# Kernel optimization log

Hardware: AMD Instinct MI355X
Metric: run time of the kernel (lower is better)

## Reference

```python
import jax, jax.numpy as jnp
import numpy as np

NUM_TEAMS = 200000
EMBED_DIM = 16
NUM_EDGES = 3200000
BATCH = 500000
EPS_NORM = 1e-12  # F.normalize clamp
EPS_SOFTMAX = 1e-16  # PyG edge-softmax denom eps
NEG_SLOPE = 0.01  # LeakyReLU default


def setup_inputs() -> dict:
    key = jax.random.key(0)
    ks = jax.random.split(key, 12)
    inp = {}
    inp["embed"] = jax.random.normal(ks[0], (NUM_TEAMS, EMBED_DIM), dtype=jnp.float32)
    inp["beta"] = jnp.ones((2,), dtype=jnp.float32)  # one learnable scalar per AGNNConv
    # torch Linear init ~ U(-1/sqrt(fan_in), 1/sqrt(fan_in)); stored as [in, out]
    def lin(k, fi, fo):
        b = 1.0 / np.sqrt(fi)
        k1, k2 = jax.random.split(k)
        return (jax.random.uniform(k1, (fi, fo), jnp.float32, -b, b),
                jax.random.uniform(k2, (fo,), jnp.float32, -b, b))
    inp["lin0_w"], inp["lin0_b"] = lin(ks[1], 2 * EMBED_DIM, 6)
    inp["lin1_w"], inp["lin1_b"] = lin(ks[2], 6, 16)
    inp["lin2_w"], inp["lin2_b"] = lin(ks[3], 16, 3)
    inp["edge_index"] = jax.random.randint(ks[4], (2, NUM_EDGES), 0, NUM_TEAMS, dtype=jnp.int64)
    inp["home"] = jax.random.randint(ks[5], (BATCH,), 0, NUM_TEAMS, dtype=jnp.int64)
    inp["away"] = jax.random.randint(ks[6], (BATCH,), 0, NUM_TEAMS, dtype=jnp.int64)
    return inp


def _agnn_conv(x, beta, src, dst, n):
    # x: [N, D]; messages flow src(j) -> dst(i); scatter-softmax over edges per dst
    xn = x / jnp.maximum(jnp.linalg.norm(x, axis=-1, keepdims=True), EPS_NORM)
    alpha = beta * jnp.sum(xn[src] * xn[dst], axis=-1)          # [E]
    m = jax.ops.segment_max(alpha, dst, num_segments=n)          # [N]
    a = jnp.exp(alpha - m[dst])                                   # [E]
    denom = jax.ops.segment_sum(a, dst, num_segments=n)          # [N]
    a = a / (denom[dst] + EPS_SOFTMAX)
    return jax.ops.segment_sum(a[:, None] * x[src], dst, num_segments=n)  # [N, D]


def _forward(embed, beta, lin0_w, lin0_b, lin1_w, lin1_b, lin2_w, lin2_b,
             src, dst, home, away):
    n = embed.shape[0]
    act = lambda v: jax.nn.leaky_relu(v, NEG_SLOPE)
    x = embed  # embedding of arange(n_teams) == the table itself
    x = act(_agnn_conv(x, beta[0], src, dst, n))
    x = act(_agnn_conv(x, beta[1], src, dst, n))
    h = jnp.concatenate([x[home], x[away]], axis=-1)  # [B, 2D]
    h = act(h @ lin0_w + lin0_b)
    h = act(h @ lin1_w + lin1_b)
    h = act(h @ lin2_w + lin2_b)
    return jax.nn.log_softmax(h, axis=0).reshape(-1, 3)  # LogSoftmax(dim=0), faithful


def reference(embed, beta, lin0_w, lin0_b, lin1_w, lin1_b, lin2_w, lin2_b,
              edge_index, home, away):
    n = embed.shape[0]
    # AGNNConv default: remove then add self-loops
    loops = jnp.arange(n, dtype=edge_index.dtype)
    mask = edge_index[0] != edge_index[1]
    safe = jnp.where(mask, edge_index[1], edge_index[0])  # self-loop-out non-loop edges
    src = jnp.concatenate([edge_index[0], loops])
    dst = jnp.concatenate([jnp.where(mask, edge_index[1], edge_index[0]), loops])
    # masked self-loops in original list become src==dst duplicates of the appended
    # self-loops only if random collision; to faithfully *remove* them we redirect
    # removed edges onto the node's own appended self-loop (alpha identical for
    # src==dst), which changes only duplicate self-loop counts with prob ~1/N.
    return _forward(embed, beta, lin0_w, lin0_b, lin1_w, lin1_b, lin2_w, lin2_b,
                    src, dst, home, away)
```

## Files before the change

### kernel.cpp

```cpp
#include <hip/hip_runtime.h>
#include <hip/hip_fp16.h>
#include <math.h>

#define TPB 256
#define NPB 512
#define NPB_SHIFT 9
#define EPB 8192
#define EPW 16
#define BCAP 12288
#define RSTRIDE 32

typedef float v2f __attribute__((ext_vector_type(2)));

__device__ __forceinline__ float leaky_relu(float v) { return v > 0.0f ? v : 0.01f * v; }

__device__ __forceinline__ float dot4(float4 a, float4 b) {
    return a.x * b.x + a.y * b.y + a.z * b.z + a.w * b.w;
}
__device__ __forceinline__ float4 f4_scale(float4 a, float s) {
    return make_float4(a.x * s, a.y * s, a.z * s, a.w * s);
}
__device__ __forceinline__ float4 f4_acc(float4 a, float w, float4 y) {
    return make_float4(fmaf(w, y.x, a.x), fmaf(w, y.y, a.y),
                       fmaf(w, y.z, a.z), fmaf(w, y.w, a.w));
}
__device__ __forceinline__ float4 f4_add_shfl(float4 v, int d) {
    return make_float4(v.x + __shfl_xor(v.x, d, 64), v.y + __shfl_xor(v.y, d, 64),
                       v.z + __shfl_xor(v.z, d, 64), v.w + __shfl_xor(v.w, d, 64));
}
__device__ __forceinline__ float4 leaky4(float4 v) {
    return make_float4(leaky_relu(v.x), leaky_relu(v.y), leaky_relu(v.z), leaky_relu(v.w));
}

__device__ __forceinline__ float4 dec4(unsigned w) {
    v2f lo = __builtin_amdgcn_cvt_pk_f32_fp8((int)w, false);
    v2f hi = __builtin_amdgcn_cvt_pk_f32_fp8((int)w, true);
    return make_float4(lo.x, lo.y, hi.x, hi.y);
}
__device__ __forceinline__ unsigned enc4(float4 v) {
    int r = __builtin_amdgcn_cvt_pk_fp8_f32(v.x, v.y, 0, false);
    r = __builtin_amdgcn_cvt_pk_fp8_f32(v.z, v.w, r, true);
    return (unsigned)r;
}

__device__ __forceinline__ void store_h4(__half* row, int l, float4 v) {
    union { float2 f; __half h[4]; } u;
    u.h[0] = __float2half(v.x); u.h[1] = __float2half(v.y);
    u.h[2] = __float2half(v.z); u.h[3] = __float2half(v.w);
    ((float2*)row)[l] = u.f;
}

__device__ __forceinline__ uint4 rec_q(const char* base, int i) {
    return *(const uint4*)(base + (size_t)i * RSTRIDE);
}
__device__ __forceinline__ float rec_n(const char* base, int i) {
    return *(const float*)(base + (size_t)i * RSTRIDE + 16);
}

__device__ __forceinline__ int wave_incl_scan(int v, int lane) {
#pragma unroll
    for (int off = 1; off < 64; off <<= 1) {
        int u = __shfl_up(v, off, 64);
        if (lane >= off) v += u;
    }
    return v;
}

__global__ void k_binA(const int* __restrict__ src, const int* __restrict__ dst,
                       unsigned* __restrict__ bdata, int* __restrict__ cbase,
                       int* __restrict__ ccnt, int E, int K,
                       const float* __restrict__ x, char* __restrict__ xqn,
                       int N) {
    __shared__ int hist[512];
    __shared__ unsigned lcol[EPB];
    __shared__ int wsum[8];
    int t = threadIdx.x;
    int lane = t & 63, wv = t >> 6;
    int c = blockIdx.x;
    int e0 = c * EPB;
    int e1 = min(e0 + EPB, E);
    int tot = e1 - e0;
    hist[t] = 0;
    __syncthreads();
    int myd[EPW], mys[EPW];
    if (tot == EPB) {
        const int4* d4 = (const int4*)(dst + e0);
        const int4* s4 = (const int4*)(src + e0);
#pragma unroll
        for (int k = 0; k < 4; ++k) {
            int4 dd = d4[t + k * 512];
            int4 ss = s4[t + k * 512];
            myd[4 * k + 0] = dd.x; myd[4 * k + 1] = dd.y;
            myd[4 * k + 2] = dd.z; myd[4 * k + 3] = dd.w;
            mys[4 * k + 0] = ss.x; mys[4 * k + 1] = ss.y;
            mys[4 * k + 2] = ss.z; mys[4 * k + 3] = ss.w;
            atomicAdd(&hist[dd.x >> NPB_SHIFT], 1);
            atomicAdd(&hist[dd.y >> NPB_SHIFT], 1);
            atomicAdd(&hist[dd.z >> NPB_SHIFT], 1);
            atomicAdd(&hist[dd.w >> NPB_SHIFT], 1);
        }
    } else {
#pragma unroll
        for (int k = 0; k < EPW; ++k) {
            int e = e0 + t + k * 512;
            int d = (e < e1) ? dst[e] : -1;
            mys[k] = (e < e1) ? src[e] : 0;
            myd[k] = d;
            if (d >= 0) atomicAdd(&hist[d >> NPB_SHIFT], 1);
        }
    }
    __syncthreads();
    int v = hist[t];
    int inc = wave_incl_scan(v, lane);
    if (lane == 63) wsum[wv] = inc;
    __syncthreads();
    if (t == 0) {
        int acc = 0;
#pragma unroll
        for (int k = 0; k < 8; ++k) { int xv = wsum[k]; wsum[k] = acc; acc += xv; }
    }
    __syncthreads();
    int excl = inc + wsum[wv] - v;
    if (t < K) {
        cbase[(size_t)c * K + t] = excl;
        ccnt[(size_t)c * K + t] = v;
    }
    __syncthreads();
    hist[t] = excl;
    __syncthreads();
    if (tot == EPB) {
#pragma unroll
        for (int k = 0; k < EPW; ++k) {
            int d = myd[k];
            int p = atomicAdd(&hist[d >> NPB_SHIFT], 1);
            lcol[p] = ((unsigned)(d & (NPB - 1)) << 18) | (unsigned)mys[k];
        }
    } else {
#pragma unroll
        for (int k = 0; k < EPW; ++k) {
            int d = myd[k];
            if (d >= 0) {
                int p = atomicAdd(&hist[d >> NPB_SHIFT], 1);
                lcol[p] = ((unsigned)(d & (NPB - 1)) << 18) | (unsigned)mys[k];
            }
        }
    }
    __syncthreads();
    unsigned* outp = bdata + (size_t)c * EPB;
    for (int i = t; i < tot; i += 512) outp[i] = lcol[i];
    int i = c * 512 + t;
    if (i < N) {
        const float4* xp = (const float4*)(x + (size_t)i * 16);
        float4 a = xp[0], b = xp[1], cc = xp[2], d = xp[3];
        float ss = dot4(a, a) + dot4(b, b) + dot4(cc, cc) + dot4(d, d);
        float nn = fmaxf(sqrtf(ss), 1e-12f);
        float inv = 1.0f / nn;
        char* rp = xqn + (size_t)i * RSTRIDE;
        *(uint4*)rp = make_uint4(enc4(f4_scale(a, inv)), enc4(f4_scale(b, inv)),
                                 enc4(f4_scale(cc, inv)), enc4(f4_scale(d, inv)));
        *(float*)(rp + 16) = nn;
    }
}

__global__ void k_binB(const unsigned* __restrict__ bdata, const int* __restrict__ cbase,
                       const int* __restrict__ ccnt,
                       int2* __restrict__ rng,
                       int* __restrict__ col, int N, int NC, int K) {
    __shared__ int cb[512];
    __shared__ int cc[512];
    __shared__ int ldeg[NPB];
    __shared__ int wsum[8];
    int b = blockIdx.x, t = threadIdx.x;
    int lane = t & 63, wv = t >> 6;
    int n0 = b << NPB_SHIFT;
    int nn = min(NPB, N - n0);
    cb[t] = (t < NC) ? cbase[(size_t)t * K + b] : 0;
    cc[t] = (t < NC) ? ccnt[(size_t)t * K + b] : 0;
    ldeg[t] = 0;
    __syncthreads();
    int mycnt = (t < NC) ? cc[t] : 0;
    const unsigned* myp = bdata + (size_t)t * EPB + cb[t];
    for (int k = 0; k < mycnt; ++k) {
        unsigned e = myp[k];
        atomicAdd(&ldeg[e >> 18], 1);
    }
    __syncthreads();
    int dv = ldeg[t];
    int inc = wave_incl_scan(dv, lane);
    if (lane == 63) wsum[wv] = inc;
    __syncthreads();
    if (t == 0) {
        int acc = 0;
#pragma unroll
        for (int k = 0; k < 8; ++k) { int xv = wsum[k]; wsum[k] = acc; acc += xv; }
    }
    __syncthreads();
    int excl = inc + wsum[wv] - dv;
    int gb = b * BCAP;
    if (t < nn) {
        rng[n0 + t] = make_int2(gb + excl, gb + excl + dv);
    }
    __syncthreads();
    ldeg[t] = excl;
    __syncthreads();
    for (int k = 0; k < mycnt; ++k) {
        unsigned e = myp[k];
        int pos = atomicAdd(&ldeg[e >> 18], 1);
        col[gb + pos] = (int)(e & 0x3FFFFu);
    }
}

__global__ void k_agnn(const char* __restrict__ xqn,
                       const int2* __restrict__ rng,
                       const int* __restrict__ col,
                       const float* __restrict__ beta_ptr, int beta_idx,
                       void* __restrict__ out, int n, int fp8_out) {
    int t = threadIdx.x;
    int l = t & 7;
    int i = blockIdx.x * (512 / 8) + (t >> 3);
    if (i >= n) return;
    float bet = beta_ptr[beta_idx];
    uint4 rowi = rec_q(xqn, i);
    float ni = rec_n(xqn, i);
    float4 x0 = dec4(rowi.x), x1 = dec4(rowi.y), x2 = dec4(rowi.z), x3 = dec4(rowi.w);
    float4 q0 = f4_scale(x0, bet), q1 = f4_scale(x1, bet),
           q2 = f4_scale(x2, bet), q3 = f4_scale(x3, bet);
    float s;
    float4 a0, a1, a2, a3;
    if (l == 0) {
        float w = __expf(bet);
        s = w;
        float wi = w * ni;
        a0 = f4_scale(x0, wi); a1 = f4_scale(x1, wi);
        a2 = f4_scale(x2, wi); a3 = f4_scale(x3, wi);
    } else {
        s = 0.0f;
        a0 = a1 = a2 = a3 = make_float4(0.f, 0.f, 0.f, 0.f);
    }
    int2 se = rng[i];
    int e1 = se.y;
    int e = se.x + l;
    uint4 rA = make_uint4(0u, 0u, 0u, 0u), rB = make_uint4(0u, 0u, 0u, 0u);
    float nA = 0.0f, nB = 0.0f;
    if (e < e1) {
        int j = col[e];
        rA = rec_q(xqn, j); nA = rec_n(xqn, j);
    }
    if (e + 8 < e1) {
        int j = col[e + 8];
        rB = rec_q(xqn, j); nB = rec_n(xqn, j);
    }
    for (; e < e1; e += 8) {
        uint4 rC = make_uint4(0u, 0u, 0u, 0u);
        float nC = 0.0f;
        if (e + 16 < e1) {
            int j = col[e + 16];
            rC = rec_q(xqn, j); nC = rec_n(xqn, j);
        }
        float4 y0 = dec4(rA.x), y1 = dec4(rA.y), y2 = dec4(rA.z), y3 = dec4(rA.w);
        float d = dot4(y0, q0) + dot4(y1, q1) + dot4(y2, q2) + dot4(y3, q3);
        float w = __expf(d);
        s += w;
        float wn = w * nA;
        a0 = f4_acc(a0, wn, y0);
        a1 = f4_acc(a1, wn, y1);
        a2 = f4_acc(a2, wn, y2);
        a3 = f4_acc(a3, wn, y3);
        rA = rB; nA = nB; rB = rC; nB = nC;
    }
#pragma unroll
    for (int d_ = 1; d_ < 8; d_ <<= 1) {
        s += __shfl_xor(s, d_, 64);
        a0 = f4_add_shfl(a0, d_);
        a1 = f4_add_shfl(a1, d_);
        a2 = f4_add_shfl(a2, d_);
        a3 = f4_add_shfl(a3, d_);
    }
    float inv = 1.0f / (s + 1e-16f);
    float4 o0 = leaky4(f4_scale(a0, inv));
    float4 o1 = leaky4(f4_scale(a1, inv));
    float4 o2 = leaky4(f4_scale(a2, inv));
    float4 o3 = leaky4(f4_scale(a3, inv));
    if (l < 4) {
        float4 oq = (l == 0) ? o0 : (l == 1) ? o1 : (l == 2) ? o2 : o3;
        if (fp8_out) {
            float ss = dot4(o0, o0) + dot4(o1, o1) + dot4(o2, o2) + dot4(o3, o3);
            float nn = fmaxf(sqrtf(ss), 1e-12f);
            char* rp = (char*)out + (size_t)i * RSTRIDE;
            ((unsigned*)rp)[l] = enc4(f4_scale(oq, 1.0f / nn));
            if (l == 0) *(float*)(rp + 16) = nn;
        } else {
            store_h4((__half*)out + (size_t)i * 16, l, oq);
        }
    }
}

__global__ void k_mlp(const __half* __restrict__ x, const int* __restrict__ home,
                      const int* __restrict__ away,
                      const float* __restrict__ w0, const float* __restrict__ b0,
                      const float* __restrict__ w1, const float* __restrict__ b1,
                      const float* __restrict__ w2, const float* __restrict__ b2,
                      float* __restrict__ z, float* __restrict__ bmax,
                      float* __restrict__ bsum, int nb) {
    __shared__ float sw0[192], sw1[96], sw2[48], sb0[6], sb1[16], sb2[3];
    __shared__ float rmax[4][3];
    __shared__ float rsum[4][3];
    int t = threadIdx.x;
    if (t < 192) sw0[t] = w0[t];
    if (t < 96)  sw1[t] = w1[t];
    if (t < 48)  sw2[t] = w2[t];
    if (t < 6)   sb0[t] = b0[t];
    if (t < 16)  sb1[t] = b1[t];
    if (t < 3)   sb2[t] = b2[t];
    __syncthreads();
    int i = blockIdx.x * blockDim.x + t;
    bool act = i < nb;
    float z0 = -3.4e38f, z1 = -3.4e38f, z2 = -3.4e38f;
    if (act) {
        float h[32];
        const uint4* hr = (const uint4*)(x + (size_t)home[i] * 16);
        const uint4* ar = (const uint4*)(x + (size_t)away[i] * 16);
        uint4 hv0 = hr[0], hv1 = hr[1];
        uint4 av0 = ar[0], av1 = ar[1];
        union { uint4 u; __half2 h2[4]; } cv;
#pragma unroll
        for (int q = 0; q < 4; ++q) {
            cv.u = (q == 0) ? hv0 : (q == 1) ? hv1 : (q == 2) ? av0 : av1;
#pragma unroll
            for (int k = 0; k < 4; ++k) {
                float2 f = __half22float2(cv.h2[k]);
                h[q * 8 + 2 * k + 0] = f.x;
                h[q * 8 + 2 * k + 1] = f.y;
            }
        }
        float t0[6];
#pragma unroll
        for (int o = 0; o < 6; ++o) {
            float acc = sb0[o];
#pragma unroll
            for (int k = 0; k < 32; ++k) acc = fmaf(h[k], sw0[k * 6 + o], acc);
            t0[o] = leaky_relu(acc);
        }
        float t1[16];
#pragma unroll
        for (int o = 0; o < 16; ++o) {
            float acc = sb1[o];
#pragma unroll
            for (int k = 0; k < 6; ++k) acc = fmaf(t0[k], sw1[k * 16 + o], acc);
            t1[o] = leaky_relu(acc);
        }
        float zz[3];
#pragma unroll
        for (int o = 0; o < 3; ++o) {
            float acc = sb2[o];
#pragma unroll
            for (int k = 0; k < 16; ++k) acc = fmaf(t1[k], sw2[k * 3 + o], acc);
            zz[o] = leaky_relu(acc);
            z[(size_t)i * 3 + o] = zz[o];
        }
        z0 = zz[0]; z1 = zz[1]; z2 = zz[2];
    }
    float w0_ = z0, w1_ = z1, w2_ = z2;
#pragma unroll
    for (int off = 32; off > 0; off >>= 1) {
        w0_ = fmaxf(w0_, __shfl_down(w0_, off));
        w1_ = fmaxf(w1_, __shfl_down(w1_, off));
        w2_ = fmaxf(w2_, __shfl_down(w2_, off));
    }
    int wid = t >> 6;
    if ((t & 63) == 0) { rmax[wid][0] = w0_; rmax[wid][1] = w1_; rmax[wid][2] = w2_; }
    __syncthreads();
    float M0 = fmaxf(fmaxf(rmax[0][0], rmax[1][0]), fmaxf(rmax[2][0], rmax[3][0]));
    float M1 = fmaxf(fmaxf(rmax[0][1], rmax[1][1]), fmaxf(rmax[2][1], rmax[3][1]));
    float M2 = fmaxf(fmaxf(rmax[0][2], rmax[1][2]), fmaxf(rmax[2][2], rmax[3][2]));
    float e0 = act ? __expf(z0 - M0) : 0.0f;
    float e1 = act ? __expf(z1 - M1) : 0.0f;
    float e2 = act ? __expf(z2 - M2) : 0.0f;
#pragma unroll
    for (int off = 32; off > 0; off >>= 1) {
        e0 += __shfl_down(e0, off);
        e1 += __shfl_down(e1, off);
        e2 += __shfl_down(e2, off);
    }
    if ((t & 63) == 0) { rsum[wid][0] = e0; rsum[wid][1] = e1; rsum[wid][2] = e2; }
    __syncthreads();
    if (t == 0) {
        float S0 = rsum[0][0] + rsum[1][0] + rsum[2][0] + rsum[3][0];
        float S1 = rsum[0][1] + rsum[1][1] + rsum[2][1] + rsum[3][1];
        float S2 = rsum[0][2] + rsum[1][2] + rsum[2][2] + rsum[3][2];
        bmax[blockIdx.x * 3 + 0] = M0; bmax[blockIdx.x * 3 + 1] = M1; bmax[blockIdx.x * 3 + 2] = M2;
        bsum[blockIdx.x * 3 + 0] = S0; bsum[blockIdx.x * 3 + 1] = S1; bsum[blockIdx.x * 3 + 2] = S2;
    }
}

__device__ __forceinline__ float pick3(int c, float L0, float L1, float L2) {
    return c == 0 ? L0 : (c == 1 ? L1 : L2);
}

__global__ void k_final(const float4* __restrict__ z4,
                        const float* __restrict__ bmax, const float* __restrict__ bsum,
                        int nblk, float4* __restrict__ out4, int n4) {
    __shared__ float lm[4][3];
    __shared__ float ls[4][3];
    __shared__ float Lsh[3];
    int t = threadIdx.x;
    float M0 = -3.4e38f, M1 = -3.4e38f, M2 = -3.4e38f;
    float S0 = 0.f, S1 = 0.f, S2 = 0.f;
    for (int b = t; b < nblk; b += 256) {
        float m0 = bmax[b * 3 + 0], s0 = bsum[b * 3 + 0];
        float n0 = fmaxf(M0, m0); S0 = S0 * __expf(M0 - n0) + s0 * __expf(m0 - n0); M0 = n0;
        float m1 = bmax[b * 3 + 1], s1 = bsum[b * 3 + 1];
        float n1 = fmaxf(M1, m1); S1 = S1 * __expf(M1 - n1) + s1 * __expf(m1 - n1); M1 = n1;
        float m2 = bmax[b * 3 + 2], s2 = bsum[b * 3 + 2];
        float n2 = fmaxf(M2, m2); S2 = S2 * __expf(M2 - n2) + s2 * __expf(m2 - n2); M2 = n2;
    }
#pragma unroll
    for (int off = 32; off > 0; off >>= 1) {
        float mo, so, nm;
        mo = __shfl_down(M0, off); so = __shfl_down(S0, off);
        nm = fmaxf(M0, mo); S0 = S0 * __expf(M0 - nm) + so * __expf(mo - nm); M0 = nm;
        mo = __shfl_down(M1, off); so = __shfl_down(S1, off);
        nm = fmaxf(M1, mo); S1 = S1 * __expf(M1 - nm) + so * __expf(mo - nm); M1 = nm;
        mo = __shfl_down(M2, off); so = __shfl_down(S2, off);
        nm = fmaxf(M2, mo); S2 = S2 * __expf(M2 - nm) + so * __expf(mo - nm); M2 = nm;
    }
    int wid = t >> 6;
    if ((t & 63) == 0) {
        lm[wid][0] = M0; lm[wid][1] = M1; lm[wid][2] = M2;
        ls[wid][0] = S0; ls[wid][1] = S1; ls[wid][2] = S2;
    }
    __syncthreads();
    if (t == 0) {
        for (int w = 1; w < 4; ++w) {
            float nm;
            nm = fmaxf(M0, lm[w][0]); S0 = S0 * __expf(M0 - nm) + ls[w][0] * __expf(lm[w][0] - nm); M0 = nm;
            nm = fmaxf(M1, lm[w][1]); S1 = S1 * __expf(M1 - nm) + ls[w][1] * __expf(lm[w][1] - nm); M1 = nm;
            nm = fmaxf(M2, lm[w][2]); S2 = S2 * __expf(M2 - nm) + ls[w][2] * __expf(lm[w][2] - nm); M2 = nm;
        }
        Lsh[0] = M0 + logf(S0);
        Lsh[1] = M1 + logf(S1);
        Lsh[2] = M2 + logf(S2);
    }
    __syncthreads();
    float L0 = Lsh[0], L1 = Lsh[1], L2 = Lsh[2];
    int i = blockIdx.x * blockDim.x + t;
    if (i >= n4) return;
    float4 v = z4[i];
    int c = i % 3;
    int c1 = (c + 1) % 3, c2 = (c + 2) % 3;
    out4[i] = make_float4(v.x - pick3(c, L0, L1, L2),
                          v.y - pick3(c1, L0, L1, L2),
                          v.z - pick3(c2, L0, L1, L2),
                          v.w - pick3(c, L0, L1, L2));
}

extern "C" void kernel_launch(void* const* d_in, const int* in_sizes, int n_in,
                              void* d_out, int out_size, void* d_ws, size_t ws_size,
                              hipStream_t stream) {
    const float* embed = (const float*)d_in[0];
    const float* beta  = (const float*)d_in[1];
    const float* w0 = (const float*)d_in[2];
    const float* b0 = (const float*)d_in[3];
    const float* w1 = (const float*)d_in[4];
    const float* b1 = (const float*)d_in[5];
    const float* w2 = (const float*)d_in[6];
    const float* b2 = (const float*)d_in[7];
    const int* eidx = (const int*)d_in[8];
    const int* home = (const int*)d_in[9];
    const int* away = (const int*)d_in[10];

    const int N = in_sizes[0] / 16;
    const int E = in_sizes[8] / 2;
    const int B = in_sizes[9];
    const int* esrc = eidx;
    const int* edst = eidx + E;
    const int K = (N + NPB - 1) >> NPB_SHIFT;
    const int NC = (E + EPB - 1) / EPB;

    char* ws = (char*)d_ws;
    size_t off = 0;
    auto alloc = [&](size_t bytes) -> char* {
        off = (off + 255) & ~(size_t)255;
        char* p = ws + off;
        off += bytes;
        return p;
    };
    size_t bdata_bytes = (size_t)NC * EPB * 4;
    size_t alias_bytes = (((size_t)N * RSTRIDE + 511) & ~(size_t)255) + (size_t)B * 3 * 4;
    char* U = alloc(bdata_bytes > alias_bytes ? bdata_bytes : alias_bytes);
    unsigned* bdata = (unsigned*)U;
    char* xqn1  = U;
    float* zbuf = (float*)(U + (((size_t)N * RSTRIDE + 511) & ~(size_t)255));

    int2* rng    = (int2*)alloc((size_t)N * 8);
    int* colw    = (int*)alloc((size_t)K * BCAP * 4);
    int* cbase   = (int*)alloc((size_t)NC * K * 4);
    int* ccnt    = (int*)alloc((size_t)NC * K * 4);
    char* xqn0   = alloc((size_t)N * RSTRIDE);
    __half* xh2  = (__half*)alloc((size_t)N * 32);
    const int nblkB = (B + TPB - 1) / TPB;
    float* bmax  = (float*)alloc((size_t)nblkB * 3 * 4);
    float* bsum  = (float*)alloc((size_t)nblkB * 3 * 4);
    (void)ws_size; (void)n_in; (void)out_size;

    k_binA<<<NC, 512, 0, stream>>>(esrc, edst, bdata, cbase, ccnt, E, K,
                                   embed, xqn0, N);
    k_binB<<<K, 512, 0, stream>>>(bdata, cbase, ccnt, rng, colw, N, NC, K);

    const int nblkN8 = (N + 63) / 64;
    k_agnn<<<nblkN8, 512, 0, stream>>>(xqn0, rng, colw, beta, 0, xqn1, N, 1);
    k_agnn<<<nblkN8, 512, 0, stream>>>(xqn1, rng, colw, beta, 1, xh2, N, 0);

    k_mlp<<<nblkB, TPB, 0, stream>>>(xh2, home, away, w0, b0, w1, b1, w2, b2,
                                     zbuf, bmax, bsum, B);
    const int n4 = (B * 3) / 4;
    k_final<<<(n4 + TPB - 1) / TPB, TPB, 0, stream>>>((const float4*)zbuf, bmax, bsum,
                                                      nblkB, (float4*)d_out, n4);
}
```

Before: 240.5 us.

## Store raw fp8 features and recompute norms on the fly in AGNN gathers

Stops storing normalized fp8 rows plus a float norm in 32-byte records. Raw features are now stored as 16-byte fp8 rows, and each gathered neighbour's inverse norm is recomputed with rsqrt inside the edge loop. This halves the bytes per random gather and the table footprint, in exchange for extra ALU per edge. The prefetch branches are replaced by clamped unconditional loads, which removes divergence but makes redundant loads at the tails. Quantizing unnormalized values to fp8 changes the precision characteristics, since the dynamic range is no longer bounded to unit vectors.

```diff
diff --git a/kernel.cpp b/kernel.cpp
--- a/kernel.cpp
+++ b/kernel.cpp
@@ -8,7 +8,6 @@
 #define EPB 8192
 #define EPW 16
 #define BCAP 12288
-#define RSTRIDE 32
 
 typedef float v2f __attribute__((ext_vector_type(2)));
 
@@ -50,13 +49,6 @@
     ((float2*)row)[l] = u.f;
 }
 
-__device__ __forceinline__ uint4 rec_q(const char* base, int i) {
-    return *(const uint4*)(base + (size_t)i * RSTRIDE);
-}
-__device__ __forceinline__ float rec_n(const char* base, int i) {
-    return *(const float*)(base + (size_t)i * RSTRIDE + 16);
-}
-
 __device__ __forceinline__ int wave_incl_scan(int v, int lane) {
 #pragma unroll
     for (int off = 1; off < 64; off <<= 1) {
@@ -69,7 +61,7 @@
 __global__ void k_binA(const int* __restrict__ src, const int* __restrict__ dst,
                        unsigned* __restrict__ bdata, int* __restrict__ cbase,
                        int* __restrict__ ccnt, int E, int K,
-                       const float* __restrict__ x, char* __restrict__ xqn,
+                       const float* __restrict__ x, uint4* __restrict__ xq,
                        int N) {
     __shared__ int hist[512];
     __shared__ unsigned lcol[EPB];
@@ -152,13 +144,7 @@
     if (i < N) {
         const float4* xp = (const float4*)(x + (size_t)i * 16);
         float4 a = xp[0], b = xp[1], cc = xp[2], d = xp[3];
-        float ss = dot4(a, a) + dot4(b, b) + dot4(cc, cc) + dot4(d, d);
-        float nn = fmaxf(sqrtf(ss), 1e-12f);
-        float inv = 1.0f / nn;
-        char* rp = xqn + (size_t)i * RSTRIDE;
-        *(uint4*)rp = make_uint4(enc4(f4_scale(a, inv)), enc4(f4_scale(b, inv)),
-                                 enc4(f4_scale(cc, inv)), enc4(f4_scale(d, inv)));
-        *(float*)(rp + 16) = nn;
+        xq[i] = make_uint4(enc4(a), enc4(b), enc4(cc), enc4(d));
     }
 }
 
@@ -210,7 +196,7 @@
     }
 }
 
-__global__ void k_agnn(const char* __restrict__ xqn,
+__global__ void k_agnn(const uint4* __restrict__ xq,
                        const int2* __restrict__ rng,
                        const int* __restrict__ col,
                        const float* __restrict__ beta_ptr, int beta_idx,
@@ -220,53 +206,46 @@
     int i = blockIdx.x * (512 / 8) + (t >> 3);
     if (i >= n) return;
     float bet = beta_ptr[beta_idx];
-    uint4 rowi = rec_q(xqn, i);
-    float ni = rec_n(xqn, i);
+    uint4 rowi = xq[i];
     float4 x0 = dec4(rowi.x), x1 = dec4(rowi.y), x2 = dec4(rowi.z), x3 = dec4(rowi.w);
-    float4 q0 = f4_scale(x0, bet), q1 = f4_scale(x1, bet),
-           q2 = f4_scale(x2, bet), q3 = f4_scale(x3, bet);
+    float sqi = dot4(x0, x0) + dot4(x1, x1) + dot4(x2, x2) + dot4(x3, x3);
+    float inv_ni = rsqrtf(fmaxf(sqi, 1e-24f));
+    float bi = bet * inv_ni;
+    float4 q0 = f4_scale(x0, bi), q1 = f4_scale(x1, bi),
+           q2 = f4_scale(x2, bi), q3 = f4_scale(x3, bi);
     float s;
     float4 a0, a1, a2, a3;
     if (l == 0) {
         float w = __expf(bet);
         s = w;
-        float wi = w * ni;
-        a0 = f4_scale(x0, wi); a1 = f4_scale(x1, wi);
-        a2 = f4_scale(x2, wi); a3 = f4_scale(x3, wi);
+        a0 = f4_scale(x0, w); a1 = f4_scale(x1, w);
+        a2 = f4_scale(x2, w); a3 = f4_scale(x3, w);
     } else {
         s = 0.0f;
         a0 = a1 = a2 = a3 = make_float4(0.f, 0.f, 0.f, 0.f);
     }
     int2 se = rng[i];
     int e1 = se.y;
+    int last = max(e1 - 1, 0);
     int e = se.x + l;
-    uint4 rA = make_uint4(0u, 0u, 0u, 0u), rB = make_uint4(0u, 0u, 0u, 0u);
-    float nA = 0.0f, nB = 0.0f;
-    if (e < e1) {
-        int j = col[e];
-        rA = rec_q(xqn, j); nA = rec_n(xqn, j);
-    }
-    if (e + 8 < e1) {
-        int j = col[e + 8];
-        rB = rec_q(xqn, j); nB = rec_n(xqn, j);
-    }
+    int j0 = min(max(col[min(e, last)], 0), n - 1);
+    uint4 rA = xq[j0];
+    int j1 = min(max(col[min(e + 8, last)], 0), n - 1);
+    uint4 rB = xq[j1];
     for (; e < e1; e += 8) {
-        uint4 rC = make_uint4(0u, 0u, 0u, 0u);
-        float nC = 0.0f;
-        if (e + 16 < e1) {
-            int j = col[e + 16];
-            rC = rec_q(xqn, j); nC = rec_n(xqn, j);
-        }
+        int j2 = min(max(col[min(e + 16, last)], 0), n - 1);
+        uint4 rC = xq[j2];
         float4 y0 = dec4(rA.x), y1 = dec4(rA.y), y2 = dec4(rA.z), y3 = dec4(rA.w);
-        float d = dot4(y0, q0) + dot4(y1, q1) + dot4(y2, q2) + dot4(y3, q3);
+        float sq = dot4(y0, y0) + dot4(y1, y1) + dot4(y2, y2) + dot4(y3, y3);
+        float inv_n = rsqrtf(fmaxf(sq, 1e-24f));
+        float d = (dot4(y0, q0) + dot4(y1, q1) + dot4(y2, q2) + dot4(y3, q3)) * inv_n;
         float w = __expf(d);
         s += w;
-        float wn = w * nA;
-        a0 = f4_acc(a0, wn, y0);
-        a1 = f4_acc(a1, wn, y1);
-        a2 = f4_acc(a2, wn, y2);
-        a3 = f4_acc(a3, wn, y3);
-        rA = rB; nA = nB; rB = rC; nB = nC;
+        a0 = f4_acc(a0, w, y0);
+        a1 = f4_acc(a1, w, y1);
+        a2 = f4_acc(a2, w, y2);
+        a3 = f4_acc(a3, w, y3);
+        rA = rB; rB = rC;
     }
 #pragma unroll
     for (int d_ = 1; d_ < 8; d_ <<= 1) {
@@ -284,11 +263,7 @@
     if (l < 4) {
         float4 oq = (l == 0) ? o0 : (l == 1) ? o1 : (l == 2) ? o2 : o3;
         if (fp8_out) {
-            float ss = dot4(o0, o0) + dot4(o1, o1) + dot4(o2, o2) + dot4(o3, o3);
-            float nn = fmaxf(sqrtf(ss), 1e-12f);
-            char* rp = (char*)out + (size_t)i * RSTRIDE;
-            ((unsigned*)rp)[l] = enc4(f4_scale(oq, 1.0f / nn));
-            if (l == 0) *(float*)(rp + 16) = nn;
+            ((unsigned*)((uint4*)out + i))[l] = enc4(oq);
         } else {
             store_h4((__half*)out + (size_t)i * 16, l, oq);
         }
@@ -486,17 +461,17 @@
         return p;
     };
     size_t bdata_bytes = (size_t)NC * EPB * 4;
-    size_t alias_bytes = (((size_t)N * RSTRIDE + 511) & ~(size_t)255) + (size_t)B * 3 * 4;
+    size_t alias_bytes = (((size_t)N * 16 + 511) & ~(size_t)255) + (size_t)B * 3 * 4;
     char* U = alloc(bdata_bytes > alias_bytes ? bdata_bytes : alias_bytes);
     unsigned* bdata = (unsigned*)U;
-    char* xqn1  = U;
-    float* zbuf = (float*)(U + (((size_t)N * RSTRIDE + 511) & ~(size_t)255));
+    uint4* xq1  = (uint4*)U;
+    float* zbuf = (float*)(U + (((size_t)N * 16 + 511) & ~(size_t)255));
 
     int2* rng    = (int2*)alloc((size_t)N * 8);
     int* colw    = (int*)alloc((size_t)K * BCAP * 4);
     int* cbase   = (int*)alloc((size_t)NC * K * 4);
     int* ccnt    = (int*)alloc((size_t)NC * K * 4);
-    char* xqn0   = alloc((size_t)N * RSTRIDE);
+    uint4* xq0   = (uint4*)alloc((size_t)N * 16);
     __half* xh2  = (__half*)alloc((size_t)N * 32);
     const int nblkB = (B + TPB - 1) / TPB;
     float* bmax  = (float*)alloc((size_t)nblkB * 3 * 4);
@@ -504,12 +479,12 @@
     (void)ws_size; (void)n_in; (void)out_size;
 
     k_binA<<<NC, 512, 0, stream>>>(esrc, edst, bdata, cbase, ccnt, E, K,
-                                   embed, xqn0, N);
+                                   embed, xq0, N);
     k_binB<<<K, 512, 0, stream>>>(bdata, cbase, ccnt, rng, colw, N, NC, K);
 
     const int nblkN8 = (N + 63) / 64;
-    k_agnn<<<nblkN8, 512, 0, stream>>>(xqn0, rng, colw, beta, 0, xqn1, N, 1);
-    k_agnn<<<nblkN8, 512, 0, stream>>>(xqn1, rng, colw, beta, 1, xh2, N, 0);
+    k_agnn<<<nblkN8, 512, 0, stream>>>(xq0, rng, colw, beta, 0, xq1, N, 1);
+    k_agnn<<<nblkN8, 512, 0, stream>>>(xq1, rng, colw, beta, 1, xh2, N, 0);
 
     k_mlp<<<nblkB, TPB, 0, stream>>>(xh2, home, away, w0, b0, w1, b1, w2, b2,
                                      zbuf, bmax, bsum, B);
```

Result: faster. 214.3 us (-10.9%).
